# Performance work log

Measured on AMD Instinct MI355X. Metric: run time of the kernel, lower is better.

## Reference

```python
import jax, jax.numpy as jnp
import numpy as np

B, N, D, H, C = 4, 1024, 768, 12, 3
Dh = D // H                      # 64
HID = int(D * 4.0 * (2.0 / 3.0)) # 2048 (SwiGLU hidden)
EPS = 1e-5


def layernorm(x, g, b):
    m = jnp.mean(x, axis=-1, keepdims=True)
    v = jnp.mean(jnp.square(x - m), axis=-1, keepdims=True)
    return (x - m) * jax.lax.rsqrt(v + EPS) * g + b


def setup_inputs() -> dict:
    key = jax.random.key(0)
    ks = jax.random.split(key, 8)
    x = jax.random.normal(ks[0], (B, N, D), jnp.float32)
    coords = jax.random.uniform(ks[1], (B, N, C), jnp.float32)
    qkv_w = jax.random.normal(ks[2], (3 * D, D), jnp.float32) * 0.02
    qkv_b = jnp.zeros((3 * D,), jnp.float32)
    rel_w = jax.random.normal(ks[3], (H, C), jnp.float32) * 0.1
    ln1_g = jnp.ones((D,), jnp.float32)
    ln1_b = jnp.zeros((D,), jnp.float32)
    ln2_g = jnp.ones((D,), jnp.float32)
    ln2_b = jnp.zeros((D,), jnp.float32)
    win_w = jax.random.normal(ks[4], (2 * HID, D), jnp.float32) * 0.02
    win_b = jnp.zeros((2 * HID,), jnp.float32)
    wout_w = jax.random.normal(ks[5], (D, HID), jnp.float32) * 0.02
    wout_b = jnp.zeros((D,), jnp.float32)
    return dict(x=x, coords=coords, ln1_g=ln1_g, ln1_b=ln1_b, qkv_w=qkv_w,
                qkv_b=qkv_b, rel_w=rel_w, ln2_g=ln2_g, ln2_b=ln2_b,
                win_w=win_w, win_b=win_b, wout_w=wout_w, wout_b=wout_b)


def reference(x, coords, ln1_g, ln1_b, qkv_w, qkv_b, rel_w, ln2_g, ln2_b,
              win_w, win_b, wout_w, wout_b):
    # --- PatchAttention on norm1(x) ---
    h = layernorm(x, ln1_g, ln1_b)
    qkv = h @ qkv_w.T + qkv_b                    # (B,N,3D)
    q, k, v = jnp.split(qkv, 3, axis=-1)

    def heads(t):  # (B,N,D) -> (B,H,N,Dh)
        return t.reshape(B, N, H, Dh).transpose(0, 2, 1, 3)

    qh, kh, vh = heads(q), heads(k), heads(v)
    scale = 1.0 / np.sqrt(Dh).astype(np.float32)
    scores = jnp.einsum('bhid,bhjd->bhij', qh, kh) * scale
    # coord bias: (coords_i - coords_j) . W_h  ==  p[b,h,i] - p[b,h,j]
    p = jnp.einsum('bnc,hc->bhn', coords, rel_w)  # (B,H,N)
    scores = scores + p[:, :, :, None] - p[:, :, None, :]
    attn = jax.nn.softmax(scores, axis=-1)
    o = jnp.einsum('bhij,bhjd->bhid', attn, vh)   # (B,H,N,Dh)
    o = o.transpose(0, 2, 1, 3).reshape(B, N, D)
    x = x + o

    # --- SwiGLU FFN on norm2(x) ---
    h2 = layernorm(x, ln2_g, ln2_b)
    uv = h2 @ win_w.T + win_b                     # (B,N,2*HID)
    u, g = jnp.split(uv, 2, axis=-1)
    act = jax.nn.silu(u) * g
    return x + act @ wout_w.T + wout_b
```

## Files before the change

### kernel.cpp

```cpp
#include <hip/hip_runtime.h>
#include <math.h>

typedef unsigned short u16;
typedef __bf16 bf16x8 __attribute__((ext_vector_type(8)));
typedef __bf16 bf16x4 __attribute__((ext_vector_type(4)));
typedef u16 u16x4 __attribute__((ext_vector_type(4)));
typedef float f32x4 __attribute__((ext_vector_type(4)));

#define NTOK 1024
#define DMODEL 768
#define NHEAD 12
#define LD3 2304
#define HIDDIM 2048

__device__ __forceinline__ float b2f(u16 u) {
  unsigned int t = ((unsigned int)u) << 16;
  float f;
  __builtin_memcpy(&f, &t, 4);
  return f;
}
__device__ __forceinline__ u16 f2b(float f) {
  unsigned int t;
  __builtin_memcpy(&t, &f, 4);
  t += 0x7fffu + ((t >> 16) & 1u);
  return (u16)(t >> 16);
}

__device__ __forceinline__ void gl_lds16(const u16* g, u16* l) {
  __builtin_amdgcn_global_load_lds(
      (__attribute__((address_space(1))) const unsigned int*)g,
      (__attribute__((address_space(3))) unsigned int*)l, 16, 0, 0);
}

__global__ __launch_bounds__(256) void signal_kernel(float* __restrict__ out,
                                                     int n, float c) {
  int i = blockIdx.x * 256 + threadIdx.x;
  if (i < n) out[i] = c;
}

__global__ __launch_bounds__(256) void detect_kernel(const u16* __restrict__ x,
                                                     int* __restrict__ flag) {
  __shared__ int cnt;
  if (threadIdx.x == 0) cnt = 0;
  __syncthreads();
  int bad = 0;
  for (int i = threadIdx.x; i < 4096; i += 256) {
    u16 v = x[2 * i];
    int e = (v >> 7) & 0xFF;
    if (e >= 0xC0) bad++;
  }
  atomicAdd(&cnt, bad);
  __syncthreads();
  if (threadIdx.x == 0) *flag = (cnt >= 64) ? 1 : 0;
}

struct CanonJobs {
  const void* s[13];
  u16* d[13];
  int n[13];
};

__global__ __launch_bounds__(256) void canon_kernel(CanonJobs jobs,
                                                    const int* __restrict__ flag) {
  int j = blockIdx.y;
  int n = jobs.n[j];
  const void* s = jobs.s[j];
  u16* d = jobs.d[j];
  bool isf32 = (*flag != 0);
  for (int i = blockIdx.x * 256 + threadIdx.x; i < n; i += gridDim.x * 256) {
    d[i] = isf32 ? f2b(((const float*)s)[i]) : ((const u16*)s)[i];
  }
}

__global__ __launch_bounds__(256) void ln_bf16_kernel(
    const u16* __restrict__ x, const u16* __restrict__ g,
    const u16* __restrict__ b, u16* __restrict__ out) {
  int row = blockIdx.x;
  int tid = threadIdx.x;
  const u16* xr = x + (size_t)row * DMODEL;
  float v0 = b2f(xr[tid]), v1 = b2f(xr[tid + 256]), v2 = b2f(xr[tid + 512]);
  float s = v0 + v1 + v2;
  float q = v0 * v0 + v1 * v1 + v2 * v2;
#pragma unroll
  for (int off = 32; off; off >>= 1) {
    s += __shfl_xor(s, off, 64);
    q += __shfl_xor(q, off, 64);
  }
  __shared__ float rs[4], rq[4];
  int wv = tid >> 6;
  if ((tid & 63) == 0) { rs[wv] = s; rq[wv] = q; }
  __syncthreads();
  s = rs[0] + rs[1] + rs[2] + rs[3];
  q = rq[0] + rq[1] + rq[2] + rq[3];
  float mean = s * (1.0f / 768.0f);
  float var = q * (1.0f / 768.0f) - mean * mean;
  float inv = rsqrtf(var + 1e-5f);
  u16* outr = out + (size_t)row * DMODEL;
  outr[tid]       = f2b((v0 - mean) * inv * b2f(g[tid])       + b2f(b[tid]));
  outr[tid + 256] = f2b((v1 - mean) * inv * b2f(g[tid + 256]) + b2f(b[tid + 256]));
  outr[tid + 512] = f2b((v2 - mean) * inv * b2f(g[tid + 512]) + b2f(b[tid + 512]));
}

__global__ __launch_bounds__(256) void ln_f32_kernel(
    const float* __restrict__ x, const u16* __restrict__ g,
    const u16* __restrict__ b, u16* __restrict__ out) {
  int row = blockIdx.x;
  int tid = threadIdx.x;
  const float* xr = x + (size_t)row * DMODEL;
  float v0 = xr[tid], v1 = xr[tid + 256], v2 = xr[tid + 512];
  float s = v0 + v1 + v2;
  float q = v0 * v0 + v1 * v1 + v2 * v2;
#pragma unroll
  for (int off = 32; off; off >>= 1) {
    s += __shfl_xor(s, off, 64);
    q += __shfl_xor(q, off, 64);
  }
  __shared__ float rs[4], rq[4];
  int wv = tid >> 6;
  if ((tid & 63) == 0) { rs[wv] = s; rq[wv] = q; }
  __syncthreads();
  s = rs[0] + rs[1] + rs[2] + rs[3];
  q = rq[0] + rq[1] + rq[2] + rq[3];
  float mean = s * (1.0f / 768.0f);
  float var = q * (1.0f / 768.0f) - mean * mean;
  float inv = rsqrtf(var + 1e-5f);
  u16* outr = out + (size_t)row * DMODEL;
  outr[tid]       = f2b((v0 - mean) * inv * b2f(g[tid])       + b2f(b[tid]));
  outr[tid + 256] = f2b((v1 - mean) * inv * b2f(g[tid + 256]) + b2f(b[tid + 256]));
  outr[tid + 512] = f2b((v2 - mean) * inv * b2f(g[tid + 512]) + b2f(b[tid + 512]));
}

__device__ __forceinline__ void gemm128_pipe(
    const u16* __restrict__ A, const u16* __restrict__ W, int K,
    int mB0, int nB0, u16* Al, u16* Bl, f32x4 (&acc)[4][4]) {
  int lane = threadIdx.x & 63;
  int wv = threadIdx.x >> 6;
  int q16 = lane & 15, quad = lane >> 4;
  int mW = (wv >> 1) * 64, nW = (wv & 1) * 64;
  int srow = lane >> 2;
  int scol = ((lane & 3) ^ ((lane >> 3) & 3)) * 8;
  int sx8 = (quad ^ ((q16 >> 1) & 3)) * 8;
  int r0 = wv * 32 + srow, r1 = r0 + 16;
  const u16* Ag0 = A + (size_t)(mB0 + r0) * K + scol;
  const u16* Ag1 = A + (size_t)(mB0 + r1) * K + scol;
  const u16* Wg0 = W + (size_t)(nB0 + r0) * K + scol;
  const u16* Wg1 = W + (size_t)(nB0 + r1) * K + scol;
  int ch0 = wv * 1024, ch1 = ch0 + 512;
  int nsteps = K >> 5;
#pragma unroll
  for (int tt = 0; tt < 2; ++tt) {
    int k0 = tt * 32;
    gl_lds16(Ag0 + k0, Al + tt * 4096 + ch0);
    gl_lds16(Wg0 + k0, Bl + tt * 4096 + ch0);
    gl_lds16(Ag1 + k0, Al + tt * 4096 + ch1);
    gl_lds16(Wg1 + k0, Bl + tt * 4096 + ch1);
  }
  int n3 = nsteps / 3;
  for (int kb = 0; kb < n3; ++kb) {
#pragma unroll
    for (int c = 0; c < 3; ++c) {
      int t = kb * 3 + c;
      if (t < nsteps - 1) asm volatile("s_waitcnt vmcnt(4)" ::: "memory");
      else                asm volatile("s_waitcnt vmcnt(0)" ::: "memory");
      __builtin_amdgcn_sched_barrier(0);
      __builtin_amdgcn_s_barrier();
      __builtin_amdgcn_sched_barrier(0);
      if (t < nsteps - 2) {
        int k0 = (t + 2) * 32;
        int bs = ((c + 2) % 3) * 4096;
        gl_lds16(Ag0 + k0, Al + bs + ch0);
        gl_lds16(Wg0 + k0, Bl + bs + ch0);
        gl_lds16(Ag1 + k0, Al + bs + ch1);
        gl_lds16(Wg1 + k0, Bl + bs + ch1);
      }
      const __bf16* Ab = (const __bf16*)(Al + c * 4096);
      const __bf16* Bb = (const __bf16*)(Bl + c * 4096);
      bf16x8 af[4], bfr[4];
#pragma unroll
      for (int si = 0; si < 4; ++si)
        af[si] = *(const bf16x8*)(Ab + (mW + si * 16 + q16) * 32 + sx8);
#pragma unroll
      for (int sj = 0; sj < 4; ++sj)
        bfr[sj] = *(const bf16x8*)(Bb + (nW + sj * 16 + q16) * 32 + sx8);
#pragma unroll
      for (int si = 0; si < 4; ++si)
#pragma unroll
        for (int sj = 0; sj < 4; ++sj)
          acc[si][sj] = __builtin_amdgcn_mfma_f32_16x16x32_bf16(af[si], bfr[sj], acc[si][sj], 0, 0, 0);
    }
  }
}

__global__ __launch_bounds__(256) void gemm_bt(
    const u16* __restrict__ Ap, const u16* __restrict__ Wp,
    const u16* __restrict__ bias, u16* __restrict__ Cp, int Nn, int K) {
  __shared__ __align__(16) u16 Al[3 * 128 * 32], Bl[3 * 128 * 32];
  int lane = threadIdx.x & 63;
  int wv = threadIdx.x >> 6;
  int q16 = lane & 15, quad = lane >> 4;
  int mBase = blockIdx.y * 128 + (wv >> 1) * 64;
  int nBase = blockIdx.x * 128 + (wv & 1) * 64;
  f32x4 acc[4][4] = {};
  gemm128_pipe(Ap, Wp, K, blockIdx.y * 128, blockIdx.x * 128, Al, Bl, acc);
#pragma unroll
  for (int si = 0; si < 4; ++si)
#pragma unroll
    for (int sj = 0; sj < 4; ++sj) {
      int col = nBase + sj * 16 + q16;
      float bcol = b2f(bias[col]);
#pragma unroll
      for (int r = 0; r < 4; ++r) {
        int rowi = mBase + si * 16 + quad * 4 + r;
        Cp[(size_t)rowi * Nn + col] = f2b(acc[si][sj][r] + bcol);
      }
    }
}

__global__ __launch_bounds__(256) void gemm_out_split(
    const u16* __restrict__ Ap, const u16* __restrict__ Wp,
    const u16* __restrict__ bias, const float* __restrict__ res,
    float* __restrict__ part, float* __restrict__ out) {
  __shared__ __align__(16) u16 Al[4 * 128 * 32], Bl[4 * 64 * 32];
  int lane = threadIdx.x & 63;
  int wv = threadIdx.x >> 6;
  int q16 = lane & 15, quad = lane >> 4;
  int mB0 = blockIdx.y * 128;
  int nB0 = blockIdx.x * 64;
  int kz = blockIdx.z;
  int kbase = kz * 1024;
  int mW = (wv >> 1) * 64, nW = (wv & 1) * 32;
  int srow = lane >> 2;
  int scol = ((lane & 3) ^ ((lane >> 3) & 3)) * 8;
  int sx8 = (quad ^ ((q16 >> 1) & 3)) * 8;
  int r0 = wv * 32 + srow, r1 = r0 + 16;
  int rb = wv * 16 + srow;
  const u16* Ag0 = Ap + (size_t)(mB0 + r0) * 2048 + kbase + scol;
  const u16* Ag1 = Ap + (size_t)(mB0 + r1) * 2048 + kbase + scol;
  const u16* Wg  = Wp + (size_t)(nB0 + rb) * 2048 + kbase + scol;
  int ch0 = wv * 1024, ch1 = ch0 + 512, chb = wv * 512;
  f32x4 acc[4][2] = {};
#pragma unroll
  for (int tt = 0; tt < 2; ++tt) {
    int k0 = tt * 32;
    gl_lds16(Ag0 + k0, Al + tt * 4096 + ch0);
    gl_lds16(Ag1 + k0, Al + tt * 4096 + ch1);
    gl_lds16(Wg + k0, Bl + tt * 2048 + chb);
  }
  for (int kb = 0; kb < 8; ++kb) {
#pragma unroll
    for (int c = 0; c < 4; ++c) {
      int t = kb * 4 + c;
      if (t < 31) asm volatile("s_waitcnt vmcnt(3)" ::: "memory");
      else        asm volatile("s_waitcnt vmcnt(0)" ::: "memory");
      __builtin_amdgcn_sched_barrier(0);
      __builtin_amdgcn_s_barrier();
      __builtin_amdgcn_sched_barrier(0);
      if (t < 30) {
        int k0 = (t + 2) * 32;
        int bs = (c + 2) & 3;
        gl_lds16(Ag0 + k0, Al + bs * 4096 + ch0);
        gl_lds16(Ag1 + k0, Al + bs * 4096 + ch1);
        gl_lds16(Wg + k0, Bl + bs * 2048 + chb);
      }
      const __bf16* Ab = (const __bf16*)(Al + c * 4096);
      const __bf16* Bb = (const __bf16*)(Bl + c * 2048);
      bf16x8 af[4], bfr[2];
#pragma unroll
      for (int si = 0; si < 4; ++si)
        af[si] = *(const bf16x8*)(Ab + (mW + si * 16 + q16) * 32 + sx8);
#pragma unroll
      for (int sj = 0; sj < 2; ++sj)
        bfr[sj] = *(const bf16x8*)(Bb + (nW + sj * 16 + q16) * 32 + sx8);
#pragma unroll
      for (int si = 0; si < 4; ++si)
#pragma unroll
        for (int sj = 0; sj < 2; ++sj)
          acc[si][sj] = __builtin_amdgcn_mfma_f32_16x16x32_bf16(af[si], bfr[sj], acc[si][sj], 0, 0, 0);
    }
  }
#pragma unroll
  for (int si = 0; si < 4; ++si)
#pragma unroll
    for (int sj = 0; sj < 2; ++sj) {
      int col = nB0 + nW + sj * 16 + q16;
#pragma unroll
      for (int r = 0; r < 4; ++r) {
        int rowi = mB0 + mW + si * 16 + quad * 4 + r;
        size_t idx = (size_t)rowi * 768 + col;
        if (kz == 0) {
          part[idx] = acc[si][sj][r];
        } else {
          out[idx] = acc[si][sj][r] + b2f(bias[col]) + res[idx];
        }
      }
    }
}

__global__ __launch_bounds__(256) void add_kernel(float* __restrict__ out,
                                                  const float* __restrict__ part) {
  int i = blockIdx.x * 256 + threadIdx.x;
  f32x4 o = ((f32x4*)out)[i];
  f32x4 p = ((const f32x4*)part)[i];
#pragma unroll
  for (int r = 0; r < 4; ++r) o[r] += p[r];
  ((f32x4*)out)[i] = o;
}

__global__ __launch_bounds__(256) void ffn_in_kernel(
    const u16* __restrict__ hp, const u16* __restrict__ Wp,
    const u16* __restrict__ bias, u16* __restrict__ actp) {
  __shared__ __align__(16) u16 Al[3 * 128 * 32], Bl[3 * 128 * 32];
  int lane = threadIdx.x & 63;
  int wv = threadIdx.x >> 6;
  int q16 = lane & 15, quad = lane >> 4;
  int mB0 = blockIdx.y * 128;
  int cB0 = blockIdx.x * 64;
  int mW = (wv >> 1) * 64;
  int cW = (wv & 1) * 32;
  int srow = lane >> 2;
  int scol = ((lane & 3) ^ ((lane >> 3) & 3)) * 8;
  int sx8 = (quad ^ ((q16 >> 1) & 3)) * 8;
  int r0 = wv * 32 + srow, r1 = r0 + 16;
  int g0 = (r0 < 64) ? (cB0 + r0) : (HIDDIM + cB0 + r0 - 64);
  int g1 = (r1 < 64) ? (cB0 + r1) : (HIDDIM + cB0 + r1 - 64);
  const u16* Ag0 = hp + (size_t)(mB0 + r0) * DMODEL + scol;
  const u16* Ag1 = hp + (size_t)(mB0 + r1) * DMODEL + scol;
  const u16* Wg0 = Wp + (size_t)g0 * DMODEL + scol;
  const u16* Wg1 = Wp + (size_t)g1 * DMODEL + scol;
  int ch0 = wv * 1024, ch1 = ch0 + 512;
  f32x4 au[4][2] = {}, ag[4][2] = {};
#pragma unroll
  for (int tt = 0; tt < 2; ++tt) {
    int k0 = tt * 32;
    gl_lds16(Ag0 + k0, Al + tt * 4096 + ch0);
    gl_lds16(Wg0 + k0, Bl + tt * 4096 + ch0);
    gl_lds16(Ag1 + k0, Al + tt * 4096 + ch1);
    gl_lds16(Wg1 + k0, Bl + tt * 4096 + ch1);
  }
  for (int kb = 0; kb < 8; ++kb) {
#pragma unroll
    for (int c = 0; c < 3; ++c) {
      int t = kb * 3 + c;
      if (t < 23) asm volatile("s_waitcnt vmcnt(4)" ::: "memory");
      else        asm volatile("s_waitcnt vmcnt(0)" ::: "memory");
      __builtin_amdgcn_sched_barrier(0);
      __builtin_amdgcn_s_barrier();
      __builtin_amdgcn_sched_barrier(0);
      if (t < 22) {
        int k0 = (t + 2) * 32;
        int bs = ((c + 2) % 3) * 4096;
        gl_lds16(Ag0 + k0, Al + bs + ch0);
        gl_lds16(Wg0 + k0, Bl + bs + ch0);
        gl_lds16(Ag1 + k0, Al + bs + ch1);
        gl_lds16(Wg1 + k0, Bl + bs + ch1);
      }
      const __bf16* Ab = (const __bf16*)(Al + c * 4096);
      const __bf16* Bb = (const __bf16*)(Bl + c * 4096);
      bf16x8 af[4], wu[2], wg[2];
#pragma unroll
      for (int si = 0; si < 4; ++si)
        af[si] = *(const bf16x8*)(Ab + (mW + si * 16 + q16) * 32 + sx8);
#pragma unroll
      for (int sj = 0; sj < 2; ++sj) {
        wu[sj] = *(const bf16x8*)(Bb + (cW + sj * 16 + q16) * 32 + sx8);
        wg[sj] = *(const bf16x8*)(Bb + (64 + cW + sj * 16 + q16) * 32 + sx8);
      }
#pragma unroll
      for (int si = 0; si < 4; ++si)
#pragma unroll
        for (int sj = 0; sj < 2; ++sj) {
          au[si][sj] = __builtin_amdgcn_mfma_f32_16x16x32_bf16(af[si], wu[sj], au[si][sj], 0, 0, 0);
          ag[si][sj] = __builtin_amdgcn_mfma_f32_16x16x32_bf16(af[si], wg[sj], ag[si][sj], 0, 0, 0);
        }
    }
  }
#pragma unroll
  for (int si = 0; si < 4; ++si)
#pragma unroll
    for (int sj = 0; sj < 2; ++sj) {
      int col = cB0 + cW + sj * 16 + q16;
      float bu = b2f(bias[col]);
      float bg = b2f(bias[HIDDIM + col]);
#pragma unroll
      for (int r = 0; r < 4; ++r) {
        int rowi = mB0 + mW + si * 16 + quad * 4 + r;
        float u = au[si][sj][r] + bu;
        float g = ag[si][sj][r] + bg;
        float s = u / (1.0f + __expf(-u));
        actp[(size_t)rowi * HIDDIM + col] = f2b(s * g);
      }
    }
}

__global__ __launch_bounds__(256) void p_kernel(
    const u16* __restrict__ coords, const u16* __restrict__ relw,
    float* __restrict__ p) {
  const float LOG2E = 1.4426950408889634f;
  int idx = blockIdx.x * 256 + threadIdx.x;
  float c0 = b2f(coords[idx * 3 + 0]);
  float c1 = b2f(coords[idx * 3 + 1]);
  float c2 = b2f(coords[idx * 3 + 2]);
  int b = idx >> 10, n = idx & 1023;
#pragma unroll
  for (int h = 0; h < NHEAD; ++h) {
    float w0 = b2f(relw[h * 3 + 0]), w1 = b2f(relw[h * 3 + 1]), w2 = b2f(relw[h * 3 + 2]);
    p[(size_t)(b * NHEAD + h) * NTOK + n] = (c0 * w0 + c1 * w1 + c2 * w2) * LOG2E;
  }
}

__global__ __launch_bounds__(256) void vt_kernel(const u16* __restrict__ qkvp,
                                                 u16* __restrict__ vtp) {
  int blk = blockIdx.x;
  int b = blk / 192;
  int rem = blk % 192;
  int h = rem >> 4;
  int nt = rem & 15;
  int wv = threadIdx.x >> 6;
  int d = threadIdx.x & 63;
  int n0 = nt * 64 + wv * 16;
  const u16* src = qkvp + ((size_t)(b * NTOK) + n0) * LD3 + 2 * DMODEL + h * 64 + d;
  u16* dst = vtp + ((size_t)((b * NHEAD + h) * 64 + d)) * NTOK + n0;
#pragma unroll
  for (int c = 0; c < 2; ++c) {
    u16 buf[8] __attribute__((aligned(16)));
#pragma unroll
    for (int i = 0; i < 8; ++i) buf[i] = src[(size_t)(c * 8 + i) * LD3];
    *(uint4*)(dst + c * 8) = *(const uint4*)buf;
  }
}

__global__ __launch_bounds__(256) void attn_kernel(
    const u16* __restrict__ qkvp, const u16* __restrict__ vtp,
    const float* __restrict__ p2, const u16* __restrict__ xp,
    float* __restrict__ x1) {
  const __bf16* qb = (const __bf16*)qkvp;
  __shared__ __align__(16) u16 Kl[4][32 * 64];
  __shared__ __align__(16) u16 Vl[4][64 * 32];
  __shared__ __align__(16) u16 Pl[4][16][40];
  __shared__ __align__(16) float Pb[1024];
  int lane = threadIdx.x & 63;
  int wv = threadIdx.x >> 6;
  int hw = blockIdx.x;
  int g = hw % 48;
  int nt = hw / 48;
  int b = g / 12, h = g % 12;
  int i0 = (nt * 4 + wv) * 16;
  int q16 = lane & 15, quad = lane >> 4;

  const float scl2 = 0.125f * 1.4426950408889634f;

  const __bf16* qrow = qb + ((size_t)(b * NTOK) + i0 + q16) * LD3 + h * 64;
  bf16x8 bq0 = *(const bf16x8*)(qrow + quad * 8);
  bf16x8 bq1 = *(const bf16x8*)(qrow + 32 + quad * 8);

  const float* prow = p2 + (size_t)(b * NHEAD + h) * NTOK;

  int krw = wv * 8 + (lane >> 3);
  int ks  = (lane & 7) ^ (krw & 7);
  const u16* kg0 = qkvp + (size_t)(b * NTOK) * LD3 + DMODEL + h * 64 + ks * 8;
  int vrw = wv * 16 + (lane >> 2);
  int vs  = (lane & 3) ^ ((vrw >> 1) & 3);
  const u16* vg0 = vtp + ((size_t)((b * NHEAD + h) * 64 + vrw)) * NTOK + vs * 8;

  int kx0 = (quad ^ (q16 & 7)) << 3;
  int kx1 = ((4 | quad) ^ (q16 & 7)) << 3;
  int vx  = (quad ^ ((q16 >> 1) & 3)) << 3;

  float mrun = -1e30f, lsum = 0.f;
  f32x4 accO[4] = {};

  gl_lds16((const u16*)(prow + wv * 256 + lane * 4), (u16*)&Pb[wv * 256]);
#pragma unroll
  for (int tt = 0; tt < 3; ++tt) {
    gl_lds16(kg0 + (size_t)(tt * 32 + krw) * LD3, &Kl[tt][wv * 512]);
    gl_lds16(vg0 + tt * 32, &Vl[tt][wv * 512]);
  }

  for (int kb = 0; kb < 8; ++kb) {
#pragma unroll
    for (int c = 0; c < 4; ++c) {
      int t = kb * 4 + c;
      if (t < 30)       asm volatile("s_waitcnt vmcnt(4)" ::: "memory");
      else if (t == 30) asm volatile("s_waitcnt vmcnt(2)" ::: "memory");
      else              asm volatile("s_waitcnt vmcnt(0)" ::: "memory");
      __builtin_amdgcn_sched_barrier(0);
      __builtin_amdgcn_s_barrier();
      __builtin_amdgcn_sched_barrier(0);
      if (t < 29) {
        int j = (t + 3) * 32;
        gl_lds16(kg0 + (size_t)(j + krw) * LD3, &Kl[(c + 3) & 3][wv * 512]);
        gl_lds16(vg0 + j, &Vl[(c + 3) & 3][wv * 512]);
      }

      int j0 = t * 32;
      const __bf16* Kb = (const __bf16*)Kl[c];
      bf16x8 ka00 = *(const bf16x8*)(Kb + q16 * 64 + kx0);
      bf16x8 ka01 = *(const bf16x8*)(Kb + q16 * 64 + kx1);
      bf16x8 ka10 = *(const bf16x8*)(Kb + (16 + q16) * 64 + kx0);
      bf16x8 ka11 = *(const bf16x8*)(Kb + (16 + q16) * 64 + kx1);
      f32x4 st0 = {}, st1 = {};
      st0 = __builtin_amdgcn_mfma_f32_16x16x32_bf16(ka00, bq0, st0, 0, 0, 0);
      st0 = __builtin_amdgcn_mfma_f32_16x16x32_bf16(ka01, bq1, st0, 0, 0, 0);
      st1 = __builtin_amdgcn_mfma_f32_16x16x32_bf16(ka10, bq0, st1, 0, 0, 0);
      st1 = __builtin_amdgcn_mfma_f32_16x16x32_bf16(ka11, bq1, st1, 0, 0, 0);

      f32x4 pjl = *(const f32x4*)(&Pb[j0 + 4 * quad]);
      f32x4 pjh = *(const f32x4*)(&Pb[j0 + 16 + 4 * quad]);
      float sl[4], sh[4];
#pragma unroll
      for (int r = 0; r < 4; ++r) {
        sl[r] = st0[r] * scl2 - pjl[r];
        sh[r] = st1[r] * scl2 - pjh[r];
      }
      float lm = fmaxf(fmaxf(fmaxf(sl[0], sl[1]), fmaxf(sl[2], sl[3])),
                       fmaxf(fmaxf(sh[0], sh[1]), fmaxf(sh[2], sh[3])));
      lm = fmaxf(lm, __shfl_xor(lm, 16, 64));
      lm = fmaxf(lm, __shfl_xor(lm, 32, 64));
      float mn = fmaxf(mrun, lm);
      float alpha = exp2f(mrun - mn);
      mrun = mn;
      float pl[4], ph[4];
#pragma unroll
      for (int r = 0; r < 4; ++r) {
        pl[r] = exp2f(sl[r] - mn);
        ph[r] = exp2f(sh[r] - mn);
      }
      float ts = (pl[0] + pl[1]) + (pl[2] + pl[3]) +
                 (ph[0] + ph[1]) + (ph[2] + ph[3]);
      ts += __shfl_xor(ts, 16, 64);
      ts += __shfl_xor(ts, 32, 64);
      lsum = lsum * alpha + ts;

      bf16x4 w0 = {(__bf16)pl[0], (__bf16)pl[1], (__bf16)pl[2], (__bf16)pl[3]};
      bf16x4 w1 = {(__bf16)ph[0], (__bf16)ph[1], (__bf16)ph[2], (__bf16)ph[3]};
      *(bf16x4*)(&Pl[wv][q16][4 * quad]) = w0;
      *(bf16x4*)(&Pl[wv][q16][16 + 4 * quad]) = w1;
      bf16x8 ap = *(const bf16x8*)(&Pl[wv][q16][quad * 8]);

      const __bf16* Vb = (const __bf16*)Vl[c];
#pragma unroll
      for (int ds = 0; ds < 4; ++ds) {
        bf16x8 av = *(const bf16x8*)(Vb + (ds * 16 + q16) * 32 + vx);
        f32x4 cc = accO[ds];
#pragma unroll
        for (int r = 0; r < 4; ++r) cc[r] *= alpha;
        accO[ds] = __builtin_amdgcn_mfma_f32_16x16x32_bf16(av, ap, cc, 0, 0, 0);
      }
    }
  }

  float rl = 1.0f / lsum;
  size_t rowbase = ((size_t)(b * NTOK) + i0 + q16) * DMODEL + h * 64;
#pragma unroll
  for (int ds = 0; ds < 4; ++ds) {
    int d0 = ds * 16 + quad * 4;
    u16x4 xv = *(const u16x4*)(xp + rowbase + d0);
    f32x4 ov;
#pragma unroll
    for (int r = 0; r < 4; ++r) ov[r] = b2f(xv[r]) + accO[ds][r] * rl;
    *(f32x4*)(x1 + rowbase + d0) = ov;
  }
}

extern "C" void kernel_launch(void* const* d_in, const int* in_sizes, int n_in,
                              void* d_out, int out_size, void* d_ws, size_t ws_size,
                              hipStream_t stream) {
  static const int esz[13] = {3145728, 12288, 768, 768, 1769472, 2304, 36,
                              768, 768, 3145728, 4096, 1572864, 768};
  float sig = -1.f;
  if (n_in != 13) {
    sig = 6000.f + 100.f * (float)n_in;
  } else {
    for (int i = 0; i < 13; ++i)
      if (in_sizes[i] != esz[i]) { sig = 1000.f + 100.f * (float)i; break; }
  }
  if (sig < 0.f && ws_size < 57258496ULL) sig = 3000.f;
  if (sig < 0.f && out_size != 3145728) sig = 3100.f;
  if (sig >= 0.f) {
    signal_kernel<<<(out_size + 255) / 256, 256, 0, stream>>>((float*)d_out, out_size, sig);
    return;
  }

  char* ws = (char*)d_ws;
  int*  flag    = (int*)ws;
  u16*  cx      = (u16*)(ws + 256);
  u16*  cqkvw   = (u16*)(ws + 6291712);
  u16*  cwinw   = (u16*)(ws + 9830656);
  u16*  cwoutw  = (u16*)(ws + 16122112);
  u16*  ccoords = (u16*)(ws + 19267840);
  u16*  cln1g   = (u16*)(ws + 19292416);
  u16*  cln1b   = (u16*)(ws + 19293952);
  u16*  cqkvb   = (u16*)(ws + 19295488);
  u16*  crelw   = (u16*)(ws + 19300096);
  u16*  cln2g   = (u16*)(ws + 19300352);
  u16*  cln2b   = (u16*)(ws + 19301888);
  u16*  cwinb   = (u16*)(ws + 19303424);
  u16*  cwoutb  = (u16*)(ws + 19311616);
  u16*  h       = (u16*)(ws + 19313152);
  u16*  qkv     = (u16*)(ws + 25604608);
  float* pbuf   = (float*)(ws + 44478976);
  float* x1     = (float*)(ws + 44675584);
  u16*  act     = qkv;
  u16*  vt      = h;
  float* part   = (float*)(ws + 256);

  detect_kernel<<<1, 256, 0, stream>>>((const u16*)d_in[0], flag);

  CanonJobs jobs;
  u16* dsts[13] = {cx, ccoords, cln1g, cln1b, cqkvw, cqkvb, crelw,
                   cln2g, cln2b, cwinw, cwinb, cwoutw, cwoutb};
  for (int i = 0; i < 13; ++i) {
    jobs.s[i] = d_in[i];
    jobs.d[i] = dsts[i];
    jobs.n[i] = in_sizes[i];
  }
  canon_kernel<<<dim3(3072, 13), 256, 0, stream>>>(jobs, flag);

  ln_bf16_kernel<<<4096, 256, 0, stream>>>(cx, cln1g, cln1b, h);
  gemm_bt<<<dim3(18, 32), 256, 0, stream>>>(h, cqkvw, cqkvb, qkv, 2304, 768);
  p_kernel<<<16, 256, 0, stream>>>(ccoords, crelw, pbuf);
  vt_kernel<<<768, 256, 0, stream>>>(qkv, vt);
  attn_kernel<<<768, 256, 0, stream>>>(qkv, vt, pbuf, cx, x1);
  ln_f32_kernel<<<4096, 256, 0, stream>>>(x1, cln2g, cln2b, h);
  ffn_in_kernel<<<dim3(32, 32), 256, 0, stream>>>(h, cwinw, cwinb, act);
  gemm_out_split<<<dim3(12, 32, 2), 256, 0, stream>>>(act, cwoutw, cwoutb, x1,
                                                      part, (float*)d_out);
  add_kernel<<<3072, 256, 0, stream>>>((float*)d_out, part);
}
```

Before: 290.3 us.

## Halve GEMM N-tiles for QKV and FFN-in, vectorize canon conversion

The QKV GEMM now uses a 128x64 tile instead of 128x128, and the FFN-in kernel a 32-column u/g tile instead of 64. Both double the grid so the 256 CUs get more blocks and better wave balance. The W-tile loads and the pipeline waitcnt values are adjusted to match. The canon conversion kernel now processes four elements per thread with vector loads and launches a smaller grid. Smaller tiles lower arithmetic intensity and reuse of the A tile, so more A traffic is re-read from L2.

```diff
diff --git a/kernel.cpp b/kernel.cpp
--- a/kernel.cpp
+++ b/kernel.cpp
@@ -63,12 +63,18 @@
 __global__ __launch_bounds__(256) void canon_kernel(CanonJobs jobs,
                                                     const int* __restrict__ flag) {
   int j = blockIdx.y;
-  int n = jobs.n[j];
+  int n4 = jobs.n[j] >> 2;
   const void* s = jobs.s[j];
   u16* d = jobs.d[j];
   bool isf32 = (*flag != 0);
-  for (int i = blockIdx.x * 256 + threadIdx.x; i < n; i += gridDim.x * 256) {
-    d[i] = isf32 ? f2b(((const float*)s)[i]) : ((const u16*)s)[i];
+  for (int i = blockIdx.x * 256 + threadIdx.x; i < n4; i += gridDim.x * 256) {
+    if (isf32) {
+      f32x4 v = *((const f32x4*)s + i);
+      u16x4 o = {f2b(v[0]), f2b(v[1]), f2b(v[2]), f2b(v[3])};
+      *((u16x4*)d + i) = o;
+    } else {
+      *((u16x4*)d + i) = *((const u16x4*)s + i);
+    }
   }
 }
 
@@ -130,87 +136,76 @@
   outr[tid + 512] = f2b((v2 - mean) * inv * b2f(g[tid + 512]) + b2f(b[tid + 512]));
 }
 
-__device__ __forceinline__ void gemm128_pipe(
-    const u16* __restrict__ A, const u16* __restrict__ W, int K,
-    int mB0, int nB0, u16* Al, u16* Bl, f32x4 (&acc)[4][4]) {
+__global__ __launch_bounds__(256) void gemm_bt(
+    const u16* __restrict__ Ap, const u16* __restrict__ Wp,
+    const u16* __restrict__ bias, u16* __restrict__ Cp, int Nn, int K) {
+  __shared__ __align__(16) u16 Al[3 * 128 * 32], Bl[3 * 64 * 32];
   int lane = threadIdx.x & 63;
   int wv = threadIdx.x >> 6;
   int q16 = lane & 15, quad = lane >> 4;
-  int mW = (wv >> 1) * 64, nW = (wv & 1) * 64;
+  int mB0 = blockIdx.y * 128;
+  int nB0 = blockIdx.x * 64;
+  int mW = (wv >> 1) * 64, nW = (wv & 1) * 32;
   int srow = lane >> 2;
   int scol = ((lane & 3) ^ ((lane >> 3) & 3)) * 8;
   int sx8 = (quad ^ ((q16 >> 1) & 3)) * 8;
   int r0 = wv * 32 + srow, r1 = r0 + 16;
-  const u16* Ag0 = A + (size_t)(mB0 + r0) * K + scol;
-  const u16* Ag1 = A + (size_t)(mB0 + r1) * K + scol;
-  const u16* Wg0 = W + (size_t)(nB0 + r0) * K + scol;
-  const u16* Wg1 = W + (size_t)(nB0 + r1) * K + scol;
-  int ch0 = wv * 1024, ch1 = ch0 + 512;
+  int rb = wv * 16 + srow;
+  const u16* Ag0 = Ap + (size_t)(mB0 + r0) * K + scol;
+  const u16* Ag1 = Ap + (size_t)(mB0 + r1) * K + scol;
+  const u16* Wg  = Wp + (size_t)(nB0 + rb) * K + scol;
+  int ch0 = wv * 1024, ch1 = ch0 + 512, chb = wv * 512;
   int nsteps = K >> 5;
+  f32x4 acc[4][2] = {};
 #pragma unroll
   for (int tt = 0; tt < 2; ++tt) {
     int k0 = tt * 32;
     gl_lds16(Ag0 + k0, Al + tt * 4096 + ch0);
-    gl_lds16(Wg0 + k0, Bl + tt * 4096 + ch0);
     gl_lds16(Ag1 + k0, Al + tt * 4096 + ch1);
-    gl_lds16(Wg1 + k0, Bl + tt * 4096 + ch1);
+    gl_lds16(Wg + k0, Bl + tt * 2048 + chb);
   }
   int n3 = nsteps / 3;
   for (int kb = 0; kb < n3; ++kb) {
 #pragma unroll
     for (int c = 0; c < 3; ++c) {
       int t = kb * 3 + c;
-      if (t < nsteps - 1) asm volatile("s_waitcnt vmcnt(4)" ::: "memory");
+      if (t < nsteps - 1) asm volatile("s_waitcnt vmcnt(3)" ::: "memory");
       else                asm volatile("s_waitcnt vmcnt(0)" ::: "memory");
       __builtin_amdgcn_sched_barrier(0);
       __builtin_amdgcn_s_barrier();
       __builtin_amdgcn_sched_barrier(0);
       if (t < nsteps - 2) {
         int k0 = (t + 2) * 32;
-        int bs = ((c + 2) % 3) * 4096;
-        gl_lds16(Ag0 + k0, Al + bs + ch0);
-        gl_lds16(Wg0 + k0, Bl + bs + ch0);
-        gl_lds16(Ag1 + k0, Al + bs + ch1);
-        gl_lds16(Wg1 + k0, Bl + bs + ch1);
+        int bs = (c + 2) % 3;
+        gl_lds16(Ag0 + k0, Al + bs * 4096 + ch0);
+        gl_lds16(Ag1 + k0, Al + bs * 4096 + ch1);
+        gl_lds16(Wg + k0, Bl + bs * 2048 + chb);
       }
       const __bf16* Ab = (const __bf16*)(Al + c * 4096);
-      const __bf16* Bb = (const __bf16*)(Bl + c * 4096);
-      bf16x8 af[4], bfr[4];
+      const __bf16* Bb = (const __bf16*)(Bl + c * 2048);
+      bf16x8 af[4], bfr[2];
 #pragma unroll
       for (int si = 0; si < 4; ++si)
         af[si] = *(const bf16x8*)(Ab + (mW + si * 16 + q16) * 32 + sx8);
 #pragma unroll
-      for (int sj = 0; sj < 4; ++sj)
+      for (int sj = 0; sj < 2; ++sj)
         bfr[sj] = *(const bf16x8*)(Bb + (nW + sj * 16 + q16) * 32 + sx8);
 #pragma unroll
       for (int si = 0; si < 4; ++si)
 #pragma unroll
-        for (int sj = 0; sj < 4; ++sj)
+        for (int sj = 0; sj < 2; ++sj)
           acc[si][sj] = __builtin_amdgcn_mfma_f32_16x16x32_bf16(af[si], bfr[sj], acc[si][sj], 0, 0, 0);
     }
   }
-}
-
-__global__ __launch_bounds__(256) void gemm_bt(
-    const u16* __restrict__ Ap, const u16* __restrict__ Wp,
-    const u16* __restrict__ bias, u16* __restrict__ Cp, int Nn, int K) {
-  __shared__ __align__(16) u16 Al[3 * 128 * 32], Bl[3 * 128 * 32];
-  int lane = threadIdx.x & 63;
-  int wv = threadIdx.x >> 6;
-  int q16 = lane & 15, quad = lane >> 4;
-  int mBase = blockIdx.y * 128 + (wv >> 1) * 64;
-  int nBase = blockIdx.x * 128 + (wv & 1) * 64;
-  f32x4 acc[4][4] = {};
-  gemm128_pipe(Ap, Wp, K, blockIdx.y * 128, blockIdx.x * 128, Al, Bl, acc);
 #pragma unroll
   for (int si = 0; si < 4; ++si)
 #pragma unroll
-    for (int sj = 0; sj < 4; ++sj) {
-      int col = nBase + sj * 16 + q16;
+    for (int sj = 0; sj < 2; ++sj) {
+      int col = nB0 + nW + sj * 16 + q16;
       float bcol = b2f(bias[col]);
 #pragma unroll
       for (int r = 0; r < 4; ++r) {
-        int rowi = mBase + si * 16 + quad * 4 + r;
+        int rowi = mB0 + mW + si * 16 + quad * 4 + r;
         Cp[(size_t)rowi * Nn + col] = f2b(acc[si][sj][r] + bcol);
       }
     }
@@ -309,87 +304,77 @@
 __global__ __launch_bounds__(256) void ffn_in_kernel(
     const u16* __restrict__ hp, const u16* __restrict__ Wp,
     const u16* __restrict__ bias, u16* __restrict__ actp) {
-  __shared__ __align__(16) u16 Al[3 * 128 * 32], Bl[3 * 128 * 32];
+  __shared__ __align__(16) u16 Al[3 * 128 * 32], Bl[3 * 64 * 32];
   int lane = threadIdx.x & 63;
   int wv = threadIdx.x >> 6;
   int q16 = lane & 15, quad = lane >> 4;
   int mB0 = blockIdx.y * 128;
-  int cB0 = blockIdx.x * 64;
+  int cB0 = blockIdx.x * 32;
   int mW = (wv >> 1) * 64;
-  int cW = (wv & 1) * 32;
+  int cW = (wv & 1) * 16;
   int srow = lane >> 2;
   int scol = ((lane & 3) ^ ((lane >> 3) & 3)) * 8;
   int sx8 = (quad ^ ((q16 >> 1) & 3)) * 8;
   int r0 = wv * 32 + srow, r1 = r0 + 16;
-  int g0 = (r0 < 64) ? (cB0 + r0) : (HIDDIM + cB0 + r0 - 64);
-  int g1 = (r1 < 64) ? (cB0 + r1) : (HIDDIM + cB0 + r1 - 64);
+  int rb = wv * 16 + srow;
+  int gb = (rb < 32) ? (cB0 + rb) : (HIDDIM + cB0 + rb - 32);
   const u16* Ag0 = hp + (size_t)(mB0 + r0) * DMODEL + scol;
   const u16* Ag1 = hp + (size_t)(mB0 + r1) * DMODEL + scol;
-  const u16* Wg0 = Wp + (size_t)g0 * DMODEL + scol;
-  const u16* Wg1 = Wp + (size_t)g1 * DMODEL + scol;
-  int ch0 = wv * 1024, ch1 = ch0 + 512;
-  f32x4 au[4][2] = {}, ag[4][2] = {};
+  const u16* Wg  = Wp + (size_t)gb * DMODEL + scol;
+  int ch0 = wv * 1024, ch1 = ch0 + 512, chb = wv * 512;
+  f32x4 au[4] = {}, ag[4] = {};
 #pragma unroll
   for (int tt = 0; tt < 2; ++tt) {
     int k0 = tt * 32;
     gl_lds16(Ag0 + k0, Al + tt * 4096 + ch0);
-    gl_lds16(Wg0 + k0, Bl + tt * 4096 + ch0);
     gl_lds16(Ag1 + k0, Al + tt * 4096 + ch1);
-    gl_lds16(Wg1 + k0, Bl + tt * 4096 + ch1);
+    gl_lds16(Wg + k0, Bl + tt * 2048 + chb);
   }
   for (int kb = 0; kb < 8; ++kb) {
 #pragma unroll
     for (int c = 0; c < 3; ++c) {
       int t = kb * 3 + c;
-      if (t < 23) asm volatile("s_waitcnt vmcnt(4)" ::: "memory");
+      if (t < 23) asm volatile("s_waitcnt vmcnt(3)" ::: "memory");
       else        asm volatile("s_waitcnt vmcnt(0)" ::: "memory");
       __builtin_amdgcn_sched_barrier(0);
       __builtin_amdgcn_s_barrier();
       __builtin_amdgcn_sched_barrier(0);
       if (t < 22) {
         int k0 = (t + 2) * 32;
-        int bs = ((c + 2) % 3) * 4096;
-        gl_lds16(Ag0 + k0, Al + bs + ch0);
-        gl_lds16(Wg0 + k0, Bl + bs + ch0);
-        gl_lds16(Ag1 + k0, Al + bs + ch1);
-        gl_lds16(Wg1 + k0, Bl + bs + ch1);
+        int bs = (c + 2) % 3;
+        gl_lds16(Ag0 + k0, Al + bs * 4096 + ch0);
+        gl_lds16(Ag1 + k0, Al + bs * 4096 + ch1);
+        gl_lds16(Wg + k0, Bl + bs * 2048 + chb);
       }
       const __bf16* Ab = (const __bf16*)(Al + c * 4096);
-      const __bf16* Bb = (const __bf16*)(Bl + c * 4096);
-      bf16x8 af[4], wu[2], wg[2];
+      const __bf16* Bb = (const __bf16*)(Bl + c * 2048);
+      bf16x8 af[4], wu, wg;
 #pragma unroll
       for (int si = 0; si < 4; ++si)
         af[si] = *(const bf16x8*)(Ab + (mW + si * 16 + q16) * 32 + sx8);
-#pragma unroll
-      for (int sj = 0; sj < 2; ++sj) {
-        wu[sj] = *(const bf16x8*)(Bb + (cW + sj * 16 + q16) * 32 + sx8);
-        wg[sj] = *(const bf16x8*)(Bb + (64 + cW + sj * 16 + q16) * 32 + sx8);
-      }
-#pragma unroll
-      for (int si = 0; si < 4; ++si)
-#pragma unroll
-        for (int sj = 0; sj < 2; ++sj) {
-          au[si][sj] = __builtin_amdgcn_mfma_f32_16x16x32_bf16(af[si], wu[sj], au[si][sj], 0, 0, 0);
-          ag[si][sj] = __builtin_amdgcn_mfma_f32_16x16x32_bf16(af[si], wg[sj], ag[si][sj], 0, 0, 0);
-        }
-    }
-  }
-#pragma unroll
-  for (int si = 0; si < 4; ++si)
-#pragma unroll
-    for (int sj = 0; sj < 2; ++sj) {
-      int col = cB0 + cW + sj * 16 + q16;
-      float bu = b2f(bias[col]);
-      float bg = b2f(bias[HIDDIM + col]);
-#pragma unroll
-      for (int r = 0; r < 4; ++r) {
-        int rowi = mB0 + mW + si * 16 + quad * 4 + r;
-        float u = au[si][sj][r] + bu;
-        float g = ag[si][sj][r] + bg;
-        float s = u / (1.0f + __expf(-u));
-        actp[(size_t)rowi * HIDDIM + col] = f2b(s * g);
-      }
-    }
+      wu = *(const bf16x8*)(Bb + (cW + q16) * 32 + sx8);
+      wg = *(const bf16x8*)(Bb + (32 + cW + q16) * 32 + sx8);
+#pragma unroll
+      for (int si = 0; si < 4; ++si) {
+        au[si] = __builtin_amdgcn_mfma_f32_16x16x32_bf16(af[si], wu, au[si], 0, 0, 0);
+        ag[si] = __builtin_amdgcn_mfma_f32_16x16x32_bf16(af[si], wg, ag[si], 0, 0, 0);
+      }
+    }
+  }
+  int col = cB0 + cW + q16;
+  float bu = b2f(bias[col]);
+  float bg = b2f(bias[HIDDIM + col]);
+#pragma unroll
+  for (int si = 0; si < 4; ++si) {
+#pragma unroll
+    for (int r = 0; r < 4; ++r) {
+      int rowi = mB0 + mW + si * 16 + quad * 4 + r;
+      float u = au[si][r] + bu;
+      float g = ag[si][r] + bg;
+      float s = u / (1.0f + __expf(-u));
+      actp[(size_t)rowi * HIDDIM + col] = f2b(s * g);
+    }
+  }
 }
 
 __global__ __launch_bounds__(256) void p_kernel(
@@ -614,15 +599,15 @@
     jobs.d[i] = dsts[i];
     jobs.n[i] = in_sizes[i];
   }
-  canon_kernel<<<dim3(3072, 13), 256, 0, stream>>>(jobs, flag);
+  canon_kernel<<<dim3(768, 13), 256, 0, stream>>>(jobs, flag);
 
   ln_bf16_kernel<<<4096, 256, 0, stream>>>(cx, cln1g, cln1b, h);
-  gemm_bt<<<dim3(18, 32), 256, 0, stream>>>(h, cqkvw, cqkvb, qkv, 2304, 768);
+  gemm_bt<<<dim3(36, 32), 256, 0, stream>>>(h, cqkvw, cqkvb, qkv, 2304, 768);
   p_kernel<<<16, 256, 0, stream>>>(ccoords, crelw, pbuf);
   vt_kernel<<<768, 256, 0, stream>>>(qkv, vt);
   attn_kernel<<<768, 256, 0, stream>>>(qkv, vt, pbuf, cx, x1);
   ln_f32_kernel<<<4096, 256, 0, stream>>>(x1, cln2g, cln2b, h);
-  ffn_in_kernel<<<dim3(32, 32), 256, 0, stream>>>(h, cwinw, cwinb, act);
+  ffn_in_kernel<<<dim3(64, 32), 256, 0, stream>>>(h, cwinw, cwinb, act);
   gemm_out_split<<<dim3(12, 32, 2), 256, 0, stream>>>(act, cwoutw, cwoutb, x1,
                                                       part, (float*)d_out);
   add_kernel<<<3072, 256, 0, stream>>>((float*)d_out, part);
```

Result: no change. 292.0 us (+0.6%).
